# Kernel tuning notes

Measured on AMD Instinct MI355X. Metric: run time of the kernel, lower is better.

Reference implementation:

```python
import jax, jax.numpy as jnp
import numpy as np

B, NPG = 128, 512            # graphs, nodes per graph (batch is contiguous & uniform)
N = B * NPG                  # 65536 nodes
DEG = 8
E = N * DEG                  # 524288 edges
F_IN, NHID = 128, 64
H, C = 3, NHID               # GAT heads, out channels per head
HC = H * C                   # 192
NCLS = 10
RATIO = 0.5
NEG_SLOPE = 0.2


def setup_inputs() -> dict:
    key = jax.random.key(0)
    ks = jax.random.split(key, 24)
    x = jax.random.normal(ks[0], (N, F_IN), jnp.float32)
    # edges constrained within each graph (graphs are contiguous blocks of NPG nodes)
    offs = jnp.repeat(jnp.arange(B, dtype=jnp.int32) * NPG, NPG * DEG)
    src = jax.random.randint(ks[1], (E,), 0, NPG, dtype=jnp.int32) + offs
    dst = jax.random.randint(ks[2], (E,), 0, NPG, dtype=jnp.int32) + offs
    edge_index = jnp.stack([src, dst], axis=0)
    edge_attr = jax.random.normal(ks[3], (E, 2), jnp.float32)
    batch = jnp.repeat(jnp.arange(B, dtype=jnp.int32), NPG)

    def lin(k, o, i):
        return jax.random.normal(k, (o, i), jnp.float32) / np.float32(np.sqrt(i))

    return {
        "x": x, "edge_index": edge_index, "edge_attr": edge_attr, "batch": batch,
        # lin: num_features -> nhid//2
        "W_lin": lin(ks[4], NHID // 2, F_IN), "b_lin": jnp.zeros((NHID // 2,), jnp.float32),
        # GATConv(nhid//2 -> nhid, heads=3, edge_dim=2)
        "W_src": lin(ks[5], HC, NHID // 2),
        "att_src": jax.random.normal(ks[6], (H, C), jnp.float32) / np.float32(np.sqrt(C)),
        "att_dst": jax.random.normal(ks[7], (H, C), jnp.float32) / np.float32(np.sqrt(C)),
        "W_edge": lin(ks[8], HC, 2),
        "att_edge": jax.random.normal(ks[9], (H, C), jnp.float32) / np.float32(np.sqrt(C)),
        "b_gat": jnp.zeros((HC,), jnp.float32),
        # SAGPool score layer: GCNConv(nhid*3 -> 1)
        "W_gcn": lin(ks[10], 1, HC), "b_gcn": jnp.zeros((1,), jnp.float32),
        # classifier MLP
        "W1": lin(ks[11], NHID, 2 * HC), "b1": jnp.zeros((NHID,), jnp.float32),
        "W2": lin(ks[12], NHID // 2, NHID), "b2": jnp.zeros((NHID // 2,), jnp.float32),
        "W3": lin(ks[13], NCLS, NHID // 2), "b3": jnp.zeros((NCLS,), jnp.float32),
    }


def reference(x, edge_index, edge_attr, batch,
              W_lin, b_lin, W_src, att_src, att_dst, W_edge, att_edge, b_gat,
              W_gcn, b_gcn, W1, b1, W2, b2, W3, b3):
    src, dst = edge_index[0], edge_index[1]

    # ---- lin + ELU -------------------------------------------------------
    h = jax.nn.elu(x @ W_lin.T + b_lin)                       # [N, nhid//2]

    # ---- GATConv(heads=3, edge_dim=2), add_self_loops fill_value='mean' --
    loop = jnp.arange(N, dtype=src.dtype)
    cnt = jax.ops.segment_sum(jnp.ones((E,), h.dtype), dst, num_segments=N)
    loop_attr = jax.ops.segment_sum(edge_attr, dst, num_segments=N) / jnp.maximum(cnt, 1.0)[:, None]
    s_full = jnp.concatenate([src, loop])
    d_full = jnp.concatenate([dst, loop])
    ea_full = jnp.concatenate([edge_attr, loop_attr], axis=0)  # [E+N, 2]

    xp = (h @ W_src.T).reshape(N, H, C)                        # projected per-head feats
    a_src = (xp * att_src).sum(-1)                             # [N, H]
    a_dst = (xp * att_dst).sum(-1)                             # [N, H]
    ef = (ea_full @ W_edge.T).reshape(-1, H, C)
    a_edge = (ef * att_edge).sum(-1)                           # [E+N, H]

    alpha = jax.nn.leaky_relu(a_src[s_full] + a_dst[d_full] + a_edge, NEG_SLOPE)
    m = jax.ops.segment_max(alpha, d_full, num_segments=N)     # scatter-softmax over dst
    ealpha = jnp.exp(alpha - m[d_full])
    denom = jax.ops.segment_sum(ealpha, d_full, num_segments=N)
    alpha = ealpha / (denom[d_full] + 1e-16)                   # [E+N, H]

    out = jax.ops.segment_sum(alpha[:, :, None] * xp[s_full], d_full, num_segments=N)
    x1 = jax.nn.relu(out.reshape(N, HC) + b_gat)               # [N, 192]

    # ---- SAGPool: GCNConv score + per-graph top-k (mask form) ------------
    xw = x1 @ W_gcn.T                                          # [N, 1]
    deg = jax.ops.segment_sum(jnp.ones((E,), x1.dtype), dst, num_segments=N) + 1.0
    dinv = jax.lax.rsqrt(deg)
    agg = jax.ops.segment_sum((dinv[src] * dinv[dst])[:, None] * xw[src], dst, num_segments=N)
    score = (agg + (dinv ** 2)[:, None] * xw + b_gcn)[:, 0]    # [N]

    k = int(np.ceil(RATIO * NPG))                              # nodes kept per graph
    s2 = score.reshape(B, NPG)
    rank = jnp.argsort(jnp.argsort(-s2, axis=1), axis=1)
    mask = rank < k                                            # [B, NPG] top-k selection

    xs = (x1 * jnp.tanh(score)[:, None]).reshape(B, NPG, HC)
    gmp = jnp.max(jnp.where(mask[:, :, None], xs, -jnp.inf), axis=1)   # [B, 192]
    gap = jnp.sum(jnp.where(mask[:, :, None], xs, 0.0), axis=1) / k    # [B, 192]
    r = jnp.concatenate([gmp, gap], axis=1)                    # [B, 384]

    # ---- classifier MLP (dropout is identity in eval) ---------------------
    r = jax.nn.relu(r @ W1.T + b1)
    r = jax.nn.relu(r @ W2.T + b2)
    return jax.nn.log_softmax(r @ W3.T + b3, axis=-1)          # [B, num_classes]
```

## Files before the change

kernel.cpp:

```cpp
#include <hip/hip_runtime.h>
#include <hip/hip_bf16.h>
#include <math.h>

#define NN   65536
#define EE   524288
#define BB   128
#define NPGC 512
#define HCC  192
#define KSEL 256
#define NEG  0.2f
#define PSEG 16
#define SEGN (NPGC / PSEG)
#define MAXD 40
#define SLOTS ((size_t)NN * MAXD)
#define EPG   4096
#define HSTR  36

__global__ __launch_bounds__(192) void k_v(
    const float* __restrict__ W_src, const float* __restrict__ att_src,
    const float* __restrict__ att_dst, const float* __restrict__ W_edge,
    const float* __restrict__ att_edge, float* __restrict__ vbuf) {
    __shared__ float red[6];
    int t = threadIdx.x;
    if (t < 6) red[t] = 0.f;
    __syncthreads();
    {
        float ae = att_edge[t];
        int h = t >> 6;
        atomicAdd(&red[h],     W_edge[2 * t]     * ae);
        atomicAdd(&red[3 + h], W_edge[2 * t + 1] * ae);
    }
    if (t < 96) {
        int h = t >> 5, k = t & 31;
        float vs = 0.f, vd = 0.f;
        for (int c = 0; c < 64; ++c) {
            float w = W_src[(h * 64 + c) * 32 + k];
            vs += w * att_src[h * 64 + c];
            vd += w * att_dst[h * 64 + c];
        }
        vbuf[t] = vs;
        vbuf[96 + t] = vd;
    }
    __syncthreads();
    if (t < 6) vbuf[192 + t] = red[t];
}

__global__ __launch_bounds__(256) void k_feat(
    const float* __restrict__ x, const float* __restrict__ W_lin,
    const float* __restrict__ b_lin, const float* __restrict__ W_src,
    const float* __restrict__ vbuf,
    float* __restrict__ xp, float* __restrict__ ap_s, float* __restrict__ ap_d) {
    __shared__ float Wl[128 * HSTR];
    __shared__ float hs[128 * HSTR];
    __shared__ float vs_s[96], vd_s[96];
    int t = threadIdx.x;
    for (int i = t; i < 4096; i += 256) {
        int j = i >> 7, k = i & 127;
        Wl[k * HSTR + j] = W_lin[i];
    }
    if (t < 96) { vs_s[t] = vbuf[t]; vd_s[t] = vbuf[96 + t]; }
    __syncthreads();
    int bx = blockIdx.x;
    int xcd = bx & 7, j2 = bx >> 3;
    int g = xcd + 8 * (j2 >> 2);
    int nb = g * NPGC + (j2 & 3) * 128;
    int nl = t >> 1, hf = t & 1;
    int n = nb + nl;
    const float4* xr = (const float4*)(x + (size_t)n * 128);
    float acc[16];
#pragma unroll
    for (int j = 0; j < 16; ++j) acc[j] = b_lin[hf * 16 + j];
#pragma unroll 8
    for (int q = 0; q < 32; ++q) {
        float4 a = xr[q];
        const float* w = &Wl[(q * 4) * HSTR + hf * 16];
#pragma unroll
        for (int j = 0; j < 16; ++j) {
            acc[j] += a.x * w[j] + a.y * w[HSTR + j] +
                      a.z * w[2 * HSTR + j] + a.w * w[3 * HSTR + j];
        }
    }
#pragma unroll
    for (int j = 0; j < 16; ++j)
        acc[j] = acc[j] > 0.f ? acc[j] : (__expf(acc[j]) - 1.f);
#pragma unroll
    for (int head = 0; head < 3; ++head) {
        float s = 0.f, d = 0.f;
#pragma unroll
        for (int j = 0; j < 16; ++j) {
            s += acc[j] * vs_s[head * 32 + hf * 16 + j];
            d += acc[j] * vd_s[head * 32 + hf * 16 + j];
        }
        s += __shfl_xor(s, 1, 64);
        d += __shfl_xor(d, 1, 64);
        if (hf == 0) {
            ap_s[(size_t)head * NN + n] = s;
            ap_d[(size_t)head * NN + n] = d;
        }
    }
    float4* hw = (float4*)&hs[nl * HSTR + hf * 16];
#pragma unroll
    for (int q = 0; q < 4; ++q)
        hw[q] = make_float4(acc[4 * q], acc[4 * q + 1],
                            acc[4 * q + 2], acc[4 * q + 3]);
    __syncthreads();
    int lane = t & 63, wave = t >> 6;
    float wreg[96];
#pragma unroll
    for (int h = 0; h < 3; ++h) {
        const float4* wp = (const float4*)(W_src + (h * 64 + lane) * 32);
#pragma unroll
        for (int q = 0; q < 8; ++q) {
            float4 w = wp[q];
            wreg[h * 32 + 4 * q]     = w.x;
            wreg[h * 32 + 4 * q + 1] = w.y;
            wreg[h * 32 + 4 * q + 2] = w.z;
            wreg[h * 32 + 4 * q + 3] = w.w;
        }
    }
    int n0 = wave * 32;
    for (int nd = 0; nd < 32; ++nd) {
        int nl2 = n0 + nd;
        const float4* hr = (const float4*)&hs[nl2 * HSTR];
        float a0 = 0.f, a1 = 0.f, a2 = 0.f;
#pragma unroll
        for (int q = 0; q < 8; ++q) {
            float4 hv = hr[q];
            a0 += hv.x*wreg[4*q] + hv.y*wreg[4*q+1] + hv.z*wreg[4*q+2] + hv.w*wreg[4*q+3];
            a1 += hv.x*wreg[32+4*q] + hv.y*wreg[32+4*q+1] + hv.z*wreg[32+4*q+2] + hv.w*wreg[32+4*q+3];
            a2 += hv.x*wreg[64+4*q] + hv.y*wreg[64+4*q+1] + hv.z*wreg[64+4*q+2] + hv.w*wreg[64+4*q+3];
        }
        size_t nbase = (size_t)(nb + nl2) * HCC;
        xp[nbase + lane] = a0;
        xp[nbase + 64 + lane] = a1;
        xp[nbase + 128 + lane] = a2;
    }
}

__global__ __launch_bounds__(1024) void k_edges(
    const int* __restrict__ ei, const float* __restrict__ ea,
    const float* __restrict__ ap_s, const float* __restrict__ ap_d,
    const float* __restrict__ vbuf,
    int* __restrict__ fill, float4* __restrict__ slotA) {
    __shared__ int   s_pos[NPGC];
    __shared__ float s_la[NPGC * 2];
    __shared__ float s_as[NPGC * 3], s_ad[NPGC * 3];
    int b = blockIdx.x, t = threadIdx.x;
    int g = (b & 7) + 8 * (b >> 3);
    int nbase = g * NPGC;
    int ebase = g * EPG;
    if (t < NPGC) s_pos[t] = 0;
    s_la[t] = 0.f;
    for (int i = t; i < NPGC * 3; i += 1024) {
        int h = i >> 9, nl = i & (NPGC - 1);
        s_as[nl * 3 + h] = ap_s[(size_t)h * NN + nbase + nl];
        s_ad[nl * 3 + h] = ap_d[(size_t)h * NN + nbase + nl];
    }
    float ac[6];
#pragma unroll
    for (int h = 0; h < 6; ++h) ac[h] = vbuf[192 + h];
    int4  se  = ((const int4*)(ei + ebase))[t];
    int4  de  = ((const int4*)(ei + EE + ebase))[t];
    float4 a0 = ((const float4*)(ea + 2 * ebase))[2 * t];
    float4 a1 = ((const float4*)(ea + 2 * ebase))[2 * t + 1];
    __syncthreads();

    int   ss[4] = {se.x, se.y, se.z, se.w};
    int   dd[4] = {de.x, de.y, de.z, de.w};
    float e0v[4] = {a0.x, a0.z, a1.x, a1.z};
    float e1v[4] = {a0.y, a0.w, a1.y, a1.w};
#pragma unroll
    for (int k = 0; k < 4; ++k) {
        int s = ss[k], d = dd[k];
        int sl = s & (NPGC - 1), dl = d & (NPGC - 1);
        float e0 = e0v[k], e1 = e1v[k];
        atomicAdd(&s_la[2 * dl],     e0);
        atomicAdd(&s_la[2 * dl + 1], e1);
        float v[3];
#pragma unroll
        for (int h = 0; h < 3; ++h) {
            float a = s_as[sl * 3 + h] + s_ad[dl * 3 + h] +
                      e0 * ac[h] + e1 * ac[3 + h];
            v[h] = a >= 0.f ? a : NEG * a;
        }
        int pos = atomicAdd(&s_pos[dl], 1);
        if (pos < MAXD - 1)
            slotA[(size_t)(nbase + dl) * MAXD + 1 + pos] =
                make_float4(v[0], v[1], v[2], __int_as_float(s));
    }
    __syncthreads();
    if (t < NPGC) {
        int cnt = s_pos[t];
        int n = nbase + t;
        fill[n] = cnt;
        float inv = 1.f / fmaxf((float)cnt, 1.f);
        float l0 = s_la[2 * t] * inv, l1 = s_la[2 * t + 1] * inv;
        float v[3];
#pragma unroll
        for (int h = 0; h < 3; ++h) {
            float a = s_as[t * 3 + h] + s_ad[t * 3 + h] +
                      l0 * ac[h] + l1 * ac[3 + h];
            v[h] = a >= 0.f ? a : NEG * a;
        }
        slotA[(size_t)n * MAXD] = make_float4(v[0], v[1], v[2],
                                              __int_as_float(n));
    }
}

__global__ __launch_bounds__(256) void k_agg(
    const int* __restrict__ fill, const float4* __restrict__ slotA,
    const float* __restrict__ xp,
    const float* __restrict__ b_gat, const float* __restrict__ W_gcn,
    float* __restrict__ x1, float* __restrict__ xwd, float* __restrict__ dinv) {
    __shared__ float2 wsl[4][3][65];
    int wave = threadIdx.x >> 6, lane = threadIdx.x & 63;
    int b = blockIdx.x;
    int xcd = b & 7, j = b >> 3;
    int g = (j >> 7) * 8 + xcd;
    int n = g * NPGC + (j & 127) * 4 + wave;

    int ctrue = fill[n];
    int cnt = ctrue < (MAXD - 1) ? ctrue : (MAXD - 1);
    int tot = cnt + 1;

    if (lane < tot) {
        float4 pk = slotA[(size_t)n * MAXD + lane];
        wsl[wave][0][lane] = make_float2(__expf(pk.x), pk.w);
        wsl[wave][1][lane] = make_float2(__expf(pk.y), pk.w);
        wsl[wave][2][lane] = make_float2(__expf(pk.z), pk.w);
    }
    bool act = lane < 48;
    int head = act ? (lane >> 4) : 0;
    const float2* wp = &wsl[wave][head][0];
    const float4* xp4 = (const float4*)xp;
    float ax = 0.f, ay = 0.f, az = 0.f, aw = 0.f, den = 0.f;
    int s = 0;
    for (; s + 3 < tot; s += 4) {
        float2 wsA = wp[s],     wsB = wp[s + 1];
        float2 wsC = wp[s + 2], wsD = wp[s + 3];
        den += (wsA.x + wsB.x) + (wsC.x + wsD.x);
        if (act) {
            float4 vA = xp4[(size_t)__float_as_int(wsA.y) * 48 + lane];
            float4 vB = xp4[(size_t)__float_as_int(wsB.y) * 48 + lane];
            float4 vC = xp4[(size_t)__float_as_int(wsC.y) * 48 + lane];
            float4 vD = xp4[(size_t)__float_as_int(wsD.y) * 48 + lane];
            ax += wsA.x * vA.x + wsB.x * vB.x + wsC.x * vC.x + wsD.x * vD.x;
            ay += wsA.x * vA.y + wsB.x * vB.y + wsC.x * vC.y + wsD.x * vD.y;
            az += wsA.x * vA.z + wsB.x * vB.z + wsC.x * vC.z + wsD.x * vD.z;
            aw += wsA.x * vA.w + wsB.x * vB.w + wsC.x * vC.w + wsD.x * vD.w;
        }
    }
    for (; s < tot; ++s) {
        float2 wsA = wp[s];
        den += wsA.x;
        if (act) {
            float4 vA = xp4[(size_t)__float_as_int(wsA.y) * 48 + lane];
            ax += wsA.x * vA.x; ay += wsA.x * vA.y;
            az += wsA.x * vA.z; aw += wsA.x * vA.w;
        }
    }
    float p = 0.f;
    if (act) {
        float id = 1.f / (den + 1e-16f);
        float4 bg = ((const float4*)b_gat)[lane];
        float4 v;
        v.x = fmaxf(ax * id + bg.x, 0.f);
        v.y = fmaxf(ay * id + bg.y, 0.f);
        v.z = fmaxf(az * id + bg.z, 0.f);
        v.w = fmaxf(aw * id + bg.w, 0.f);
        ((float4*)x1)[(size_t)n * 48 + lane] = v;
        float4 wg = ((const float4*)W_gcn)[lane];
        p = v.x * wg.x + v.y * wg.y + v.z * wg.z + v.w * wg.w;
    }
#pragma unroll
    for (int msk = 32; msk > 0; msk >>= 1) p += __shfl_xor(p, msk, 64);
    if (lane == 0) {
        float dv = rsqrtf((float)ctrue + 1.f);
        xwd[n] = p * dv;
        dinv[n] = dv;
    }
}

__global__ __launch_bounds__(256) void k_score(
    const int* __restrict__ fill, const float4* __restrict__ slotA,
    const float* __restrict__ xwd, const float* __restrict__ dinv,
    const float* __restrict__ b_gcn, float* __restrict__ score) {
    int wave = threadIdx.x >> 6, lane = threadIdx.x & 63;
    int b = blockIdx.x;
    int xcd = b & 7, j = b >> 3;
    int g = (j >> 7) * 8 + xcd;
    int n = g * NPGC + (j & 127) * 4 + wave;

    int ctrue = fill[n];
    int cnt = ctrue < (MAXD - 1) ? ctrue : (MAXD - 1);
    float acc = 0.f;
    if (lane <= cnt) {
        int src = __float_as_int(
            ((const float*)slotA)[((size_t)n * MAXD + lane) * 4 + 3]);
        acc = xwd[src];
    }
#pragma unroll
    for (int msk = 32; msk > 0; msk >>= 1) acc += __shfl_xor(acc, msk, 64);
    if (lane == 0) score[n] = b_gcn[0] + dinv[n] * acc;
}

__global__ __launch_bounds__(192) void k_poolrank(
    const float* __restrict__ score, const float* __restrict__ x1,
    float* __restrict__ pmax, float* __restrict__ psum) {
    __shared__ float sc[NPGC];
    __shared__ float ts_s[SEGN];
    __shared__ int sel_s[SEGN];
    int b = blockIdx.x;
    int xcd = b & 7, gslot = (b >> 3) & 15, seg = b >> 7;
    int g = gslot * 8 + xcd;
    int t = threadIdx.x;
    int gbase = g * NPGC;
    for (int i = t; i < NPGC; i += 192) sc[i] = score[gbase + i];
    __syncthreads();
    if (t < SEGN) {
        int iloc = seg * SEGN + t;
        float si = sc[iloc];
        int rank = 0;
        for (int j = 0; j < NPGC; ++j) {
            float sj = sc[j];
            rank += (sj > si) || (sj == si && j < iloc);
        }
        sel_s[t] = (rank < KSEL) ? 1 : 0;
        ts_s[t] = tanhf(si);
    }
    __syncthreads();
    int nb = gbase + seg * SEGN;
    float mx = -1e30f, sm = 0.f;
    for (int i = 0; i < SEGN; ++i) {
        if (sel_s[i]) {
            float v = x1[(size_t)(nb + i) * HCC + t] * ts_s[i];
            mx = fmaxf(mx, v);
            sm += v;
        }
    }
    size_t pb = (size_t)(g * PSEG + seg) * HCC + t;
    pmax[pb] = mx;
    psum[pb] = sm;
}

__global__ __launch_bounds__(384) void k_mlp(
    const float* __restrict__ pmax, const float* __restrict__ psum,
    const float* __restrict__ W1, const float* __restrict__ b1,
    const float* __restrict__ W2, const float* __restrict__ b2,
    const float* __restrict__ W3, const float* __restrict__ b3,
    float* __restrict__ out) {
    __shared__ float rs[384], part[384], h1[64], h2[32], lg[10], mls;
    int g = blockIdx.x, t = threadIdx.x;
    if (t < HCC) {
        float mx = -1e30f, sm = 0.f;
#pragma unroll
        for (int s = 0; s < PSEG; ++s) {
            mx = fmaxf(mx, pmax[(size_t)(g * PSEG + s) * HCC + t]);
            sm += psum[(size_t)(g * PSEG + s) * HCC + t];
        }
        rs[t] = mx;
        rs[HCC + t] = sm * (1.f / (float)KSEL);
    }
    __syncthreads();
    {
        int o = t / 6, sl = t - o * 6;
        const float* wr = W1 + o * 384 + sl * 64;
        const float* rr = rs + sl * 64;
        float s = 0.f;
#pragma unroll 8
        for (int k = 0; k < 64; ++k) s += rr[k] * wr[k];
        part[t] = s;
    }
    __syncthreads();
    if (t < 64) {
        float s = b1[t];
#pragma unroll
        for (int j = 0; j < 6; ++j) s += part[t * 6 + j];
        h1[t] = fmaxf(s, 0.f);
    }
    __syncthreads();
    if (t < 256) {
        int o = t >> 3, sl = t & 7;
        const float* wr = W2 + o * 64 + sl * 8;
        const float* hr = h1 + sl * 8;
        float s = 0.f;
#pragma unroll
        for (int k = 0; k < 8; ++k) s += hr[k] * wr[k];
        part[t] = s;
    }
    __syncthreads();
    if (t < 32) {
        float s = b2[t];
#pragma unroll
        for (int j = 0; j < 8; ++j) s += part[t * 8 + j];
        h2[t] = fmaxf(s, 0.f);
    }
    __syncthreads();
    if (t < 10) {
        float s = b3[t];
        for (int k = 0; k < 32; ++k) s += h2[k] * W3[t * 32 + k];
        lg[t] = s;
    }
    __syncthreads();
    if (t == 0) {
        float mx = lg[0];
        for (int j = 1; j < 10; ++j) mx = fmaxf(mx, lg[j]);
        float se = 0.f;
        for (int j = 0; j < 10; ++j) se += expf(lg[j] - mx);
        mls = mx + logf(se);
    }
    __syncthreads();
    if (t < 10) out[g * 10 + t] = lg[t] - mls;
}

extern "C" void kernel_launch(void* const* d_in, const int* in_sizes, int n_in,
                              void* d_out, int out_size, void* d_ws, size_t ws_size,
                              hipStream_t stream) {
    const float* x        = (const float*)d_in[0];
    const int*   ei       = (const int*)d_in[1];
    const float* ea       = (const float*)d_in[2];
    const float* W_lin    = (const float*)d_in[4];
    const float* b_lin    = (const float*)d_in[5];
    const float* W_src    = (const float*)d_in[6];
    const float* att_src  = (const float*)d_in[7];
    const float* att_dst  = (const float*)d_in[8];
    const float* W_edge   = (const float*)d_in[9];
    const float* att_edge = (const float*)d_in[10];
    const float* b_gat    = (const float*)d_in[11];
    const float* W_gcn    = (const float*)d_in[12];
    const float* b_gcn    = (const float*)d_in[13];
    const float* W1 = (const float*)d_in[14]; const float* b1 = (const float*)d_in[15];
    const float* W2 = (const float*)d_in[16]; const float* b2 = (const float*)d_in[17];
    const float* W3 = (const float*)d_in[18]; const float* b3 = (const float*)d_in[19];
    float* out = (float*)d_out;

    char* ws = (char*)d_ws;
    size_t off = 0;
    auto alloc = [&](size_t bytes) {
        size_t r = off;
        off += (bytes + 255) & ~(size_t)255;
        return r;
    };
    float* xp      = (float*)(ws + alloc((size_t)NN * HCC * 4));
    float* x1      = (float*)(ws + alloc((size_t)NN * HCC * 4));
    int*   fill    = (int*)(ws + alloc((size_t)NN * 4));
    float* ap_s    = (float*)(ws + alloc((size_t)NN * 3 * 4));
    float* ap_d    = (float*)(ws + alloc((size_t)NN * 3 * 4));
    float4* slotA  = (float4*)(ws + alloc(SLOTS * 16));
    float* xwd     = (float*)(ws + alloc((size_t)NN * 4));
    float* dinv    = (float*)(ws + alloc((size_t)NN * 4));
    float* score   = (float*)(ws + alloc((size_t)NN * 4));
    float* vbuf    = (float*)(ws + alloc(256 * 4));
    float* pmax    = (float*)(ws + alloc((size_t)BB * PSEG * HCC * 4));
    float* psum    = (float*)(ws + alloc((size_t)BB * PSEG * HCC * 4));

    k_v<<<1, 192, 0, stream>>>(W_src, att_src, att_dst, W_edge, att_edge, vbuf);
    k_feat<<<512, 256, 0, stream>>>(x, W_lin, b_lin, W_src, vbuf,
                                    xp, ap_s, ap_d);
    k_edges<<<BB, 1024, 0, stream>>>(ei, ea, ap_s, ap_d, vbuf, fill, slotA);
    k_agg<<<NN / 4, 256, 0, stream>>>(fill, slotA, xp, b_gat, W_gcn,
                                      x1, xwd, dinv);
    k_score<<<NN / 4, 256, 0, stream>>>(fill, slotA, xwd, dinv, b_gcn, score);
    k_poolrank<<<BB * PSEG, 192, 0, stream>>>(score, x1, pmax, psum);
    k_mlp<<<BB, 384, 0, stream>>>(pmax, psum, W1, b1, W2, b2, W3, b3, out);
}
```

Measured before the change: 243.7 us.

## Fuse top-k pooling and classifier MLP into one per-graph kernel

Merges the segmented pooling/rank kernel and the MLP kernel into a single kernel with one 512-thread block per graph. Each thread ranks one node, then 384 threads pool over two halves of the nodes and reduce in shared memory before the MLP. This removes a launch and the global partial max/sum buffers. In exchange, it cuts the pooling grid from 2048 blocks to 128, so each thread runs a long serial loop over 256 nodes with less parallelism for memory reads.

```diff
diff --git a/kernel.cpp b/kernel.cpp
--- a/kernel.cpp
+++ b/kernel.cpp
@@ -9,8 +9,6 @@
 #define HCC  192
 #define KSEL 256
 #define NEG  0.2f
-#define PSEG 16
-#define SEGN (NPGC / PSEG)
 #define MAXD 40
 #define SLOTS ((size_t)NN * MAXD)
 #define EPG   4096
@@ -304,65 +302,56 @@
     if (lane == 0) score[n] = b_gcn[0] + dinv[n] * acc;
 }
 
-__global__ __launch_bounds__(192) void k_poolrank(
+__global__ __launch_bounds__(512) void k_poolmlp(
     const float* __restrict__ score, const float* __restrict__ x1,
-    float* __restrict__ pmax, float* __restrict__ psum) {
-    __shared__ float sc[NPGC];
-    __shared__ float ts_s[SEGN];
-    __shared__ int sel_s[SEGN];
-    int b = blockIdx.x;
-    int xcd = b & 7, gslot = (b >> 3) & 15, seg = b >> 7;
-    int g = gslot * 8 + xcd;
-    int t = threadIdx.x;
-    int gbase = g * NPGC;
-    for (int i = t; i < NPGC; i += 192) sc[i] = score[gbase + i];
-    __syncthreads();
-    if (t < SEGN) {
-        int iloc = seg * SEGN + t;
-        float si = sc[iloc];
-        int rank = 0;
-        for (int j = 0; j < NPGC; ++j) {
-            float sj = sc[j];
-            rank += (sj > si) || (sj == si && j < iloc);
-        }
-        sel_s[t] = (rank < KSEL) ? 1 : 0;
-        ts_s[t] = tanhf(si);
-    }
-    __syncthreads();
-    int nb = gbase + seg * SEGN;
-    float mx = -1e30f, sm = 0.f;
-    for (int i = 0; i < SEGN; ++i) {
-        if (sel_s[i]) {
-            float v = x1[(size_t)(nb + i) * HCC + t] * ts_s[i];
-            mx = fmaxf(mx, v);
-            sm += v;
-        }
-    }
-    size_t pb = (size_t)(g * PSEG + seg) * HCC + t;
-    pmax[pb] = mx;
-    psum[pb] = sm;
-}
-
-__global__ __launch_bounds__(384) void k_mlp(
-    const float* __restrict__ pmax, const float* __restrict__ psum,
     const float* __restrict__ W1, const float* __restrict__ b1,
     const float* __restrict__ W2, const float* __restrict__ b2,
     const float* __restrict__ W3, const float* __restrict__ b3,
     float* __restrict__ out) {
+    __shared__ float sc[NPGC];
+    __shared__ float ts_s[NPGC];
+    __shared__ int   sel_s[NPGC];
+    __shared__ float pmx[2][HCC], psm[2][HCC];
     __shared__ float rs[384], part[384], h1[64], h2[32], lg[10], mls;
-    int g = blockIdx.x, t = threadIdx.x;
+    int b = blockIdx.x;
+    int g = (b & 7) + 8 * (b >> 3);
+    int t = threadIdx.x;
+    int gbase = g * NPGC;
+    sc[t] = score[gbase + t];
+    __syncthreads();
+    {
+        float si = sc[t];
+        int rank = 0;
+        for (int j = 0; j < NPGC; ++j) {
+            float sj = sc[j];
+            rank += (sj > si) || (sj == si && j < t);
+        }
+        sel_s[t] = (rank < KSEL) ? 1 : 0;
+        ts_s[t] = tanhf(si);
+    }
+    __syncthreads();
+    if (t < 384) {
+        int ch = t % HCC, half = t / HCC;
+        int nA = half * 256;
+        float mx = -1e30f, sm = 0.f;
+        for (int i = 0; i < 256; ++i) {
+            int node = nA + i;
+            if (sel_s[node]) {
+                float v = x1[(size_t)(gbase + node) * HCC + ch] * ts_s[node];
+                mx = fmaxf(mx, v);
+                sm += v;
+            }
+        }
+        pmx[half][ch] = mx;
+        psm[half][ch] = sm;
+    }
+    __syncthreads();
     if (t < HCC) {
-        float mx = -1e30f, sm = 0.f;
-#pragma unroll
-        for (int s = 0; s < PSEG; ++s) {
-            mx = fmaxf(mx, pmax[(size_t)(g * PSEG + s) * HCC + t]);
-            sm += psum[(size_t)(g * PSEG + s) * HCC + t];
-        }
-        rs[t] = mx;
-        rs[HCC + t] = sm * (1.f / (float)KSEL);
-    }
-    __syncthreads();
-    {
+        rs[t] = fmaxf(pmx[0][t], pmx[1][t]);
+        rs[HCC + t] = (psm[0][t] + psm[1][t]) * (1.f / (float)KSEL);
+    }
+    __syncthreads();
+    if (t < 384) {
         int o = t / 6, sl = t - o * 6;
         const float* wr = W1 + o * 384 + sl * 64;
         const float* rr = rs + sl * 64;
@@ -451,8 +440,6 @@
     float* dinv    = (float*)(ws + alloc((size_t)NN * 4));
     float* score   = (float*)(ws + alloc((size_t)NN * 4));
     float* vbuf    = (float*)(ws + alloc(256 * 4));
-    float* pmax    = (float*)(ws + alloc((size_t)BB * PSEG * HCC * 4));
-    float* psum    = (float*)(ws + alloc((size_t)BB * PSEG * HCC * 4));
 
     k_v<<<1, 192, 0, stream>>>(W_src, att_src, att_dst, W_edge, att_edge, vbuf);
     k_feat<<<512, 256, 0, stream>>>(x, W_lin, b_lin, W_src, vbuf,
@@ -461,6 +448,5 @@
     k_agg<<<NN / 4, 256, 0, stream>>>(fill, slotA, xp, b_gat, W_gcn,
                                       x1, xwd, dinv);
     k_score<<<NN / 4, 256, 0, stream>>>(fill, slotA, xwd, dinv, b_gcn, score);
-    k_poolrank<<<BB * PSEG, 192, 0, stream>>>(score, x1, pmax, psum);
-    k_mlp<<<BB, 384, 0, stream>>>(pmax, psum, W1, b1, W2, b2, W3, b3, out);
-}
+    k_poolmlp<<<BB, 512, 0, stream>>>(score, x1, W1, b1, W2, b2, W3, b3, out);
+}
```

Measured after the change: 274.2 us. +12.5%, slower.
